# Kernel tuning notes

Hardware: AMD Instinct MI355X
Metric: run time of the kernel (lower is better)

The kernel has to match this reference:

```python
import jax, jax.numpy as jnp
import numpy as np

HEAD_DIM = 128
HIDDEN = 2048
MAX_SEQ = 2048
NUM_HEADS = 16
NUM_KV_HEADS = 8
NUM_LAYERS = 32
LAYER_IDX = 5
SCALE = 1.0 / HEAD_DIM ** 0.5
N_REP = NUM_HEADS // NUM_KV_HEADS


def setup_inputs() -> dict:
    key = jax.random.key(0)
    ks = jax.random.split(key, 6)
    x = jax.random.normal(ks[0], (1, HIDDEN, 1, 1), jnp.float32)
    kv_cache = jax.random.normal(ks[1], (2 * NUM_LAYERS, NUM_KV_HEADS, MAX_SEQ, HEAD_DIM), jnp.float32)
    q_w = jax.random.normal(ks[2], (NUM_HEADS * HEAD_DIM, HIDDEN), jnp.float32) * 0.02
    k_w = jax.random.normal(ks[3], (NUM_KV_HEADS * HEAD_DIM, HIDDEN), jnp.float32) * 0.02
    v_w = jax.random.normal(ks[4], (NUM_KV_HEADS * HEAD_DIM, HIDDEN), jnp.float32) * 0.02
    o_w = jax.random.normal(ks[5], (HIDDEN, NUM_HEADS * HEAD_DIM), jnp.float32) * 0.02
    return {"x": x, "kv_cache": kv_cache, "q_w": q_w, "k_w": k_w, "v_w": v_w,
            "o_w": o_w, "current_pos": 1024}


def reference(x, kv_cache, q_w, k_w, v_w, o_w, current_pos):
    # 1x1 Conv2d on [1, C, 1, 1] == matrix-vector product
    xv = x.reshape(HIDDEN)
    q = (q_w @ xv).reshape(NUM_HEADS, HEAD_DIM)        # [H, D]
    k = (k_w @ xv).reshape(NUM_KV_HEADS, HEAD_DIM)     # [KV, D]
    v = (v_w @ xv).reshape(NUM_KV_HEADS, HEAD_DIM)     # [KV, D]

    k_idx = 2 * LAYER_IDX
    v_idx = k_idx + 1
    # functional slice-write of the new token's K/V into the cache
    kv_cache = kv_cache.at[k_idx, :, current_pos, :].set(k)
    kv_cache = kv_cache.at[v_idx, :, current_pos, :].set(v)

    k_full = kv_cache[k_idx]   # [KV, S, D]
    v_full = kv_cache[v_idx]   # [KV, S, D]

    # GQA: q head h uses kv head h // N_REP (matches repeat+view in torch)
    qg = q.reshape(NUM_KV_HEADS, N_REP, HEAD_DIM)                     # [KV, R, D]
    scores = jnp.einsum('grd,gsd->grs', qg, k_full) * SCALE           # [KV, R, S]
    probs = jax.nn.softmax(scores, axis=-1)
    attn = jnp.einsum('grs,gsd->grd', probs, v_full)                  # [KV, R, D]
    attn = attn.reshape(NUM_HEADS * HEAD_DIM)

    out = (o_w @ attn).reshape(1, HIDDEN, 1, 1)
    return out
```

## Files before the change

kernel.cpp:

```cpp
#include <hip/hip_runtime.h>

#define HEAD_DIM   128
#define HIDDEN     2048
#define MAX_SEQ    2048
#define NUM_HEADS  16
#define NUM_KV     8
#define LAYER_IDX  5
#define NSPLIT     16
#define CHUNK      128
#define SCALE      0.08838834764831845f

#define WS_Q     0
#define WS_K     2048
#define WS_V     3072
#define WS_LP    4096
#define WS_OP    4352

__device__ __forceinline__ float wave_reduce_sum(float v) {
    #pragma unroll
    for (int off = 32; off > 0; off >>= 1) v += __shfl_xor(v, off);
    return v;
}

__global__ __launch_bounds__(256) void qkv_kernel(const float* __restrict__ x,
                                                  const float* __restrict__ q_w,
                                                  const float* __restrict__ k_w,
                                                  const float* __restrict__ v_w,
                                                  float* __restrict__ ws) {
    const int t  = threadIdx.x;
    const int r0 = blockIdx.x * 4;
    float4 x0 = ((const float4*)x)[t];
    float4 x1 = ((const float4*)x)[t + 256];

    const float* w0; int obase; float s_out;
    if (r0 < 2048)      { w0 = q_w + (size_t)r0 * HIDDEN;          obase = WS_Q + r0;          s_out = SCALE; }
    else if (r0 < 3072) { w0 = k_w + (size_t)(r0 - 2048) * HIDDEN; obase = WS_K + (r0 - 2048); s_out = 1.0f; }
    else                { w0 = v_w + (size_t)(r0 - 3072) * HIDDEN; obase = WS_V + (r0 - 3072); s_out = 1.0f; }

    float p[4];
    #pragma unroll
    for (int r = 0; r < 4; ++r) {
        const float* w = w0 + (size_t)r * HIDDEN;
        float4 a0 = ((const float4*)w)[t];
        float4 a1 = ((const float4*)w)[t + 256];
        p[r] = a0.x * x0.x + a0.y * x0.y + a0.z * x0.z + a0.w * x0.w
             + a1.x * x1.x + a1.y * x1.y + a1.z * x1.z + a1.w * x1.w;
    }
    #pragma unroll
    for (int r = 0; r < 4; ++r) p[r] = wave_reduce_sum(p[r]);

    __shared__ float red[4][4];
    const int wave = t >> 6, lane = t & 63;
    if (lane == 0) {
        #pragma unroll
        for (int r = 0; r < 4; ++r) red[r][wave] = p[r];
    }
    __syncthreads();
    if (t < 4) ws[obase + t] = (red[t][0] + red[t][1] + red[t][2] + red[t][3]) * s_out;
}

__global__ __launch_bounds__(256) void attn_kernel(const float* __restrict__ kv_cache,
                                                   const float* __restrict__ wsq,
                                                   const int* __restrict__ cur_pos,
                                                   float* __restrict__ lp,
                                                   float* __restrict__ op) {
    const int g     = blockIdx.x;
    const int split = blockIdx.y;
    const int s0    = split * CHUNK;
    const int cpos  = *cur_pos;
    const int t     = threadIdx.x;
    const int wave  = t >> 6, lane = t & 63;

    const float* kbase = kv_cache + ((size_t)(2 * LAYER_IDX)     * NUM_KV + g) * (size_t)MAX_SEQ * HEAD_DIM;
    const float* vbase = kv_cache + ((size_t)(2 * LAYER_IDX + 1) * NUM_KV + g) * (size_t)MAX_SEQ * HEAD_DIM;
    const float* knew  = wsq + WS_K + g * HEAD_DIM;
    const float* vnew  = wsq + WS_V + g * HEAD_DIM;

    __shared__ float4 ktile[CHUNK * 32];
    __shared__ float  sc[2][CHUNK];
    __shared__ float4 smv[2][8][32];
    __shared__ float  lred[2][2];
    __shared__ float  lsum[2];

    float4 kreg[16];
    #pragma unroll
    for (int i = 0; i < 16; ++i) {
        const int idx = i * 256 + t;
        const int row = idx >> 5, col = idx & 31;
        const int s = s0 + row;
        const float4* src = (s == cpos) ? (const float4*)knew
                                        : (const float4*)(kbase + (size_t)s * HEAD_DIM);
        kreg[i] = src[col];
    }

    const int vd4 = t & 31, vsub = t >> 5;
    float4 vreg[16];
    #pragma unroll
    for (int i = 0; i < 16; ++i) {
        const int j = i * 8 + vsub;
        const int s = s0 + j;
        const float* vrow = (s == cpos) ? vnew : (vbase + (size_t)s * HEAD_DIM);
        vreg[i] = ((const float4*)vrow)[vd4];
    }

    #pragma unroll
    for (int i = 0; i < 16; ++i) ktile[i * 256 + t] = kreg[i];
    __syncthreads();

    const int dq = lane & 3;
    {
        const float4* q04 = (const float4*)(wsq + WS_Q + (g * 2 + 0) * HEAD_DIM);
        const float4* q14 = (const float4*)(wsq + WS_Q + (g * 2 + 1) * HEAD_DIM);
        float4 q0s[8], q1s[8];
        #pragma unroll
        for (int r = 0; r < 8; ++r) { q0s[r] = q04[dq * 8 + r]; q1s[r] = q14[dq * 8 + r]; }

        #pragma unroll
        for (int p = 0; p < 2; ++p) {
            const int pos = p * 64 + wave * 16 + (lane >> 2);
            float a0 = 0.f, a1 = 0.f;
            #pragma unroll
            for (int r = 0; r < 8; ++r) {
                float4 kk = ktile[pos * 32 + dq * 8 + r];
                a0 += q0s[r].x * kk.x + q0s[r].y * kk.y + q0s[r].z * kk.z + q0s[r].w * kk.w;
                a1 += q1s[r].x * kk.x + q1s[r].y * kk.y + q1s[r].z * kk.z + q1s[r].w * kk.w;
            }
            a0 += __shfl_xor(a0, 1); a0 += __shfl_xor(a0, 2);
            a1 += __shfl_xor(a1, 1); a1 += __shfl_xor(a1, 2);
            if (dq == 0) { sc[0][pos] = a0; sc[1][pos] = a1; }
        }
    }
    __syncthreads();

    if (t < 128) {
        float e0 = __expf(sc[0][t]);
        float e1 = __expf(sc[1][t]);
        sc[0][t] = e0; sc[1][t] = e1;
        float w0 = wave_reduce_sum(e0);
        float w1 = wave_reduce_sum(e1);
        if (lane == 0) { lred[0][wave] = w0; lred[1][wave] = w1; }
    }
    __syncthreads();
    if (t == 0) {
        lsum[0] = lred[0][0] + lred[0][1];
        lsum[1] = lred[1][0] + lred[1][1];
    }

    {
        float4 a0 = {0.f,0.f,0.f,0.f}, a1 = {0.f,0.f,0.f,0.f};
        #pragma unroll
        for (int i = 0; i < 16; ++i) {
            const int j = i * 8 + vsub;
            const float e0 = sc[0][j], e1 = sc[1][j];
            const float4 vv = vreg[i];
            a0.x += e0 * vv.x; a0.y += e0 * vv.y; a0.z += e0 * vv.z; a0.w += e0 * vv.w;
            a1.x += e1 * vv.x; a1.y += e1 * vv.y; a1.z += e1 * vv.z; a1.w += e1 * vv.w;
        }
        smv[0][vsub][vd4] = a0;
        smv[1][vsub][vd4] = a1;
    }
    __syncthreads();
    if (t < 64) {
        const int rep = t >> 5, q4 = t & 31;
        float4 s = smv[rep][0][q4];
        #pragma unroll
        for (int r = 1; r < 8; ++r) {
            float4 b = smv[rep][r][q4];
            s.x += b.x; s.y += b.y; s.z += b.z; s.w += b.w;
        }
        const int h = g * 2 + rep;
        ((float4*)(op + ((size_t)(h * NSPLIT + split)) * HEAD_DIM))[q4] = s;
    }
    if (t == 0) {
        lp[(g * 2 + 0) * NSPLIT + split] = lsum[0];
        lp[(g * 2 + 1) * NSPLIT + split] = lsum[1];
    }
}

__global__ __launch_bounds__(256) void out_kernel(const float* __restrict__ o_w,
                                                  const float* __restrict__ lp,
                                                  const float* __restrict__ op,
                                                  float* __restrict__ out) {
    const int t = threadIdx.x;
    __shared__ float  linv[NUM_HEADS];
    __shared__ float4 attn_s[512];
    __shared__ float  red[8][4];

    if (t < NUM_HEADS) {
        float l = 0.f;
        #pragma unroll
        for (int s = 0; s < NSPLIT; ++s) l += lp[t * NSPLIT + s];
        linv[t] = 1.0f / l;
    }
    __syncthreads();

    const float4* op4 = (const float4*)op;
    #pragma unroll
    for (int k = 0; k < 2; ++k) {
        const int fi = t + 256 * k;
        const int h = fi >> 5, d4 = fi & 31;
        float4 acc = {0.f,0.f,0.f,0.f};
        #pragma unroll
        for (int s = 0; s < NSPLIT; ++s) {
            float4 v = op4[(h * NSPLIT + s) * 32 + d4];
            acc.x += v.x; acc.y += v.y; acc.z += v.z; acc.w += v.w;
        }
        const float li = linv[h];
        acc.x *= li; acc.y *= li; acc.z *= li; acc.w *= li;
        attn_s[fi] = acc;
    }
    __syncthreads();

    const int row0 = blockIdx.x * 8;
    float4 xa0 = attn_s[t];
    float4 xa1 = attn_s[t + 256];

    float p[8];
    #pragma unroll
    for (int r = 0; r < 8; ++r) {
        const float* w = o_w + (size_t)(row0 + r) * HIDDEN;
        float4 a0 = ((const float4*)w)[t];
        float4 a1 = ((const float4*)w)[t + 256];
        p[r] = a0.x * xa0.x + a0.y * xa0.y + a0.z * xa0.z + a0.w * xa0.w
             + a1.x * xa1.x + a1.y * xa1.y + a1.z * xa1.z + a1.w * xa1.w;
    }
    #pragma unroll
    for (int r = 0; r < 8; ++r) p[r] = wave_reduce_sum(p[r]);

    const int wave = t >> 6, lane = t & 63;
    if (lane == 0) {
        #pragma unroll
        for (int r = 0; r < 8; ++r) red[r][wave] = p[r];
    }
    __syncthreads();
    if (t < 8) out[row0 + t] = red[t][0] + red[t][1] + red[t][2] + red[t][3];
}

extern "C" void kernel_launch(void* const* d_in, const int* in_sizes, int n_in,
                              void* d_out, int out_size, void* d_ws, size_t ws_size,
                              hipStream_t stream) {
    const float* x    = (const float*)d_in[0];
    const float* kv   = (const float*)d_in[1];
    const float* q_w  = (const float*)d_in[2];
    const float* k_w  = (const float*)d_in[3];
    const float* v_w  = (const float*)d_in[4];
    const float* o_w  = (const float*)d_in[5];
    const int*   cpos = (const int*)d_in[6];
    float* ws  = (float*)d_ws;
    float* out = (float*)d_out;

    qkv_kernel<<<1024, 256, 0, stream>>>(x, q_w, k_w, v_w, ws);
    attn_kernel<<<dim3(NUM_KV, NSPLIT), 256, 0, stream>>>(kv, ws, cpos, ws + WS_LP, ws + WS_OP);
    out_kernel<<<256, 256, 0, stream>>>(o_w, ws + WS_LP, ws + WS_OP, out);
}
```

Baseline: 25.25 us.

## Split attention blocks per query head instead of per KV head

The attention grid changes from one block per KV group to one block per query head, doubling the block count from 128 to 256. Each block now scores and accumulates for a single query head, which shortens per-block compute and raises parallelism across CUs. In exchange, every K/V chunk is read from global memory twice, once by each of the two heads sharing the group, doubling KV cache traffic.

Result: slower. 26.21 us (+3.8%).

```diff
diff --git a/kernel.cpp b/kernel.cpp
--- a/kernel.cpp
+++ b/kernel.cpp
@@ -64,7 +64,8 @@
                                                    const int* __restrict__ cur_pos,
                                                    float* __restrict__ lp,
                                                    float* __restrict__ op) {
-    const int g     = blockIdx.x;
+    const int h     = blockIdx.x;
+    const int g     = h >> 1;
     const int split = blockIdx.y;
     const int s0    = split * CHUNK;
     const int cpos  = *cur_pos;
@@ -77,10 +78,10 @@
     const float* vnew  = wsq + WS_V + g * HEAD_DIM;
 
     __shared__ float4 ktile[CHUNK * 32];
-    __shared__ float  sc[2][CHUNK];
-    __shared__ float4 smv[2][8][32];
-    __shared__ float  lred[2][2];
-    __shared__ float  lsum[2];
+    __shared__ float  sc[CHUNK];
+    __shared__ float4 smv[8][32];
+    __shared__ float  lred[2];
+    __shared__ float  lsum;
 
     float4 kreg[16];
     #pragma unroll
@@ -109,72 +110,58 @@
 
     const int dq = lane & 3;
     {
-        const float4* q04 = (const float4*)(wsq + WS_Q + (g * 2 + 0) * HEAD_DIM);
-        const float4* q14 = (const float4*)(wsq + WS_Q + (g * 2 + 1) * HEAD_DIM);
-        float4 q0s[8], q1s[8];
-        #pragma unroll
-        for (int r = 0; r < 8; ++r) { q0s[r] = q04[dq * 8 + r]; q1s[r] = q14[dq * 8 + r]; }
+        const float4* q4p = (const float4*)(wsq + WS_Q + h * HEAD_DIM);
+        float4 qs[8];
+        #pragma unroll
+        for (int r = 0; r < 8; ++r) qs[r] = q4p[dq * 8 + r];
 
         #pragma unroll
         for (int p = 0; p < 2; ++p) {
             const int pos = p * 64 + wave * 16 + (lane >> 2);
-            float a0 = 0.f, a1 = 0.f;
+            float a0 = 0.f;
             #pragma unroll
             for (int r = 0; r < 8; ++r) {
                 float4 kk = ktile[pos * 32 + dq * 8 + r];
-                a0 += q0s[r].x * kk.x + q0s[r].y * kk.y + q0s[r].z * kk.z + q0s[r].w * kk.w;
-                a1 += q1s[r].x * kk.x + q1s[r].y * kk.y + q1s[r].z * kk.z + q1s[r].w * kk.w;
+                a0 += qs[r].x * kk.x + qs[r].y * kk.y + qs[r].z * kk.z + qs[r].w * kk.w;
             }
             a0 += __shfl_xor(a0, 1); a0 += __shfl_xor(a0, 2);
-            a1 += __shfl_xor(a1, 1); a1 += __shfl_xor(a1, 2);
-            if (dq == 0) { sc[0][pos] = a0; sc[1][pos] = a1; }
+            if (dq == 0) sc[pos] = a0;
         }
     }
     __syncthreads();
 
     if (t < 128) {
-        float e0 = __expf(sc[0][t]);
-        float e1 = __expf(sc[1][t]);
-        sc[0][t] = e0; sc[1][t] = e1;
-        float w0 = wave_reduce_sum(e0);
-        float w1 = wave_reduce_sum(e1);
-        if (lane == 0) { lred[0][wave] = w0; lred[1][wave] = w1; }
-    }
-    __syncthreads();
-    if (t == 0) {
-        lsum[0] = lred[0][0] + lred[0][1];
-        lsum[1] = lred[1][0] + lred[1][1];
-    }
+        float e = __expf(sc[t]);
+        sc[t] = e;
+        float w = wave_reduce_sum(e);
+        if (lane == 0) lred[wave] = w;
+    }
+    __syncthreads();
+    if (t == 0) lsum = lred[0] + lred[1];
 
     {
-        float4 a0 = {0.f,0.f,0.f,0.f}, a1 = {0.f,0.f,0.f,0.f};
+        float4 a = {0.f,0.f,0.f,0.f};
         #pragma unroll
         for (int i = 0; i < 16; ++i) {
             const int j = i * 8 + vsub;
-            const float e0 = sc[0][j], e1 = sc[1][j];
+            const float e = sc[j];
             const float4 vv = vreg[i];
-            a0.x += e0 * vv.x; a0.y += e0 * vv.y; a0.z += e0 * vv.z; a0.w += e0 * vv.w;
-            a1.x += e1 * vv.x; a1.y += e1 * vv.y; a1.z += e1 * vv.z; a1.w += e1 * vv.w;
-        }
-        smv[0][vsub][vd4] = a0;
-        smv[1][vsub][vd4] = a1;
-    }
-    __syncthreads();
-    if (t < 64) {
-        const int rep = t >> 5, q4 = t & 31;
-        float4 s = smv[rep][0][q4];
+            a.x += e * vv.x; a.y += e * vv.y; a.z += e * vv.z; a.w += e * vv.w;
+        }
+        smv[vsub][vd4] = a;
+    }
+    __syncthreads();
+    if (t < 32) {
+        const int q4 = t;
+        float4 s = smv[0][q4];
         #pragma unroll
         for (int r = 1; r < 8; ++r) {
-            float4 b = smv[rep][r][q4];
+            float4 b = smv[r][q4];
             s.x += b.x; s.y += b.y; s.z += b.z; s.w += b.w;
         }
-        const int h = g * 2 + rep;
         ((float4*)(op + ((size_t)(h * NSPLIT + split)) * HEAD_DIM))[q4] = s;
     }
-    if (t == 0) {
-        lp[(g * 2 + 0) * NSPLIT + split] = lsum[0];
-        lp[(g * 2 + 1) * NSPLIT + split] = lsum[1];
-    }
+    if (t == 0) lp[h * NSPLIT + split] = lsum;
 }
 
 __global__ __launch_bounds__(256) void out_kernel(const float* __restrict__ o_w,
@@ -250,6 +237,6 @@
     float* out = (float*)d_out;
 
     qkv_kernel<<<1024, 256, 0, stream>>>(x, q_w, k_w, v_w, ws);
-    attn_kernel<<<dim3(NUM_KV, NSPLIT), 256, 0, stream>>>(kv, ws, cpos, ws + WS_LP, ws + WS_OP);
+    attn_kernel<<<dim3(NUM_HEADS, NSPLIT), 256, 0, stream>>>(kv, ws, cpos, ws + WS_LP, ws + WS_OP);
     out_kernel<<<256, 256, 0, stream>>>(o_w, ws + WS_LP, ws + WS_OP, out);
 }
```
